# Optimization experiments

Measured on AMD Instinct MI355X. Metric: run time of the kernel, lower is better.

The kernel has to match this reference:

```python
import jax, jax.numpy as jnp
import numpy as np

W_DIM = 512
CHANNELS = 1024
SIZE = 64            # H = W = 64
SAMPLING_RATE = 64.0
BANDWIDTH = 2.0


def setup_inputs() -> dict:
    key = jax.random.key(0)
    k_w, k_f, k_p, k_wt, k_aw = jax.random.split(key, 5)
    B = 16
    w = jax.random.normal(k_w, (B, W_DIM), dtype=jnp.float32)
    # freqs init as in SynthesisInput.__init__
    freqs = jax.random.normal(k_f, (CHANNELS, 2), dtype=jnp.float32)
    radii = jnp.sqrt(jnp.sum(freqs ** 2, axis=1, keepdims=True))
    freqs = freqs / (radii * jnp.exp(radii ** 2) ** 0.25) * BANDWIDTH
    phases = jax.random.uniform(k_p, (CHANNELS,), dtype=jnp.float32) - 0.5
    weight = jax.random.normal(k_wt, (CHANNELS, CHANNELS), dtype=jnp.float32)
    # affine FC layer (weight_init=0 in original; use small random for a useful test)
    affine_w = jax.random.normal(k_aw, (4, W_DIM), dtype=jnp.float32) * 0.1
    affine_b = jnp.array([1.0, 0.0, 0.0, 0.0], dtype=jnp.float32)
    return {"w": w, "freqs": freqs, "phases": phases, "weight": weight,
            "affine_w": affine_w, "affine_b": affine_b}


def _forward(w, freqs, phases, weight, affine_w, affine_b):
    B = w.shape[0]
    C = freqs.shape[0]
    H = Wd = SIZE
    # affine: FullyConnectedLayer gain = 1/sqrt(in_features)
    t = w @ affine_w.T / jnp.sqrt(jnp.float32(W_DIM)) + affine_b  # [B,4]
    t = t / jnp.linalg.norm(t[:, :2], axis=1, keepdims=True)
    c, s = t[:, 0], t[:, 1]
    # rotation block of m_r (identity base transform, so transform_ = m_r @ m_t)
    R = jnp.stack([jnp.stack([c, -s], -1), jnp.stack([s, c], -1)], -2)  # [B,2,2]
    # translation column: transform_[:, :2, 2] = R @ (-t[:,2:4])
    trans_col = -jnp.einsum('bij,bj->bi', R, t[:, 2:4])                 # [B,2]
    phases_b = phases[None, :] + jnp.einsum('cd,bd->bc', freqs, trans_col)  # [B,C]
    freqs_b = jnp.einsum('cd,bde->bce', freqs, R)                           # [B,C,2]
    amps = jnp.clip(
        1.0 - (jnp.linalg.norm(freqs_b, axis=2) - BANDWIDTH)
        / (SAMPLING_RATE / 2 - BANDWIDTH), 0.0, 1.0)                        # [B,C]
    # affine_grid (align_corners=False): normalized coords (2i+1)/N - 1, scaled
    sx = 0.5 * Wd / SAMPLING_RATE
    sy = 0.5 * H / SAMPLING_RATE
    u = ((jnp.arange(Wd, dtype=jnp.float32) + 0.5) / Wd * 2.0 - 1.0) * sx  # x (width)
    v = ((jnp.arange(H, dtype=jnp.float32) + 0.5) / H * 2.0 - 1.0) * sy    # y (height)
    grid = jnp.stack(jnp.meshgrid(u, v, indexing='xy'), axis=-1)           # [H,W,2]
    x = jnp.einsum('hwd,bcd->bhwc', grid, freqs_b) + phases_b[:, None, None, :]
    x = jnp.sin(x * (2.0 * jnp.pi)) * amps[:, None, None, :]
    x = jnp.einsum('bhwc,kc->bhwk', x, weight / jnp.sqrt(jnp.float32(C)))
    return jnp.transpose(x, (0, 3, 1, 2))  # [B,C,H,W]


def reference(w, freqs, phases, weight, affine_w, affine_b):
    return _forward(w, freqs, phases, weight, affine_w, affine_b)
```

## Files before the change

### kernel.cpp

```cpp
#include <hip/hip_runtime.h>

typedef __attribute__((ext_vector_type(4))) float f32x4;
typedef __attribute__((ext_vector_type(8))) short s16x8;
typedef __attribute__((ext_vector_type(8))) unsigned short u16x8;

#define W_DIM   512
#define CHANNELS 1024
#define SPATIAL 4096
#define NB      16

__device__ inline unsigned short f2bf(float x){
  unsigned int u = __float_as_uint(x);
  u += 0x7fffu + ((u >> 16) & 1u);
  return (unsigned short)(u >> 16);
}

__device__ inline float sin2pi(float x){
  return __builtin_amdgcn_sinf(__builtin_amdgcn_fractf(x));
}
__device__ inline float cos2pi(float x){
  return __builtin_amdgcn_cosf(__builtin_amdgcn_fractf(x));
}

__device__ inline void async_load16(const unsigned short* g, unsigned short* l){
  __builtin_amdgcn_global_load_lds(
      (const __attribute__((address_space(1))) void*)g,
      (__attribute__((address_space(3))) void*)l, 16, 0, 0);
}

__global__ void sy_setup(const float* __restrict__ w, const float* __restrict__ freqs,
                         const float* __restrict__ phases, const float* __restrict__ affine_w,
                         const float* __restrict__ affine_b, float4* __restrict__ params){
  int b = blockIdx.x;
  int t = threadIdx.x;
  float p0=0.f, p1=0.f, p2=0.f, p3=0.f;
  #pragma unroll
  for (int it = 0; it < 2; ++it){
    int i = t + it*256;
    float wv = w[b*W_DIM + i];
    p0 += wv * affine_w[0*W_DIM + i];
    p1 += wv * affine_w[1*W_DIM + i];
    p2 += wv * affine_w[2*W_DIM + i];
    p3 += wv * affine_w[3*W_DIM + i];
  }
  #pragma unroll
  for (int off = 32; off >= 1; off >>= 1){
    p0 += __shfl_down(p0, off);
    p1 += __shfl_down(p1, off);
    p2 += __shfl_down(p2, off);
    p3 += __shfl_down(p3, off);
  }
  __shared__ float red[4][4];
  __shared__ float sc[4];
  int wave = t >> 6, lane = t & 63;
  if (lane == 0){ red[wave][0]=p0; red[wave][1]=p1; red[wave][2]=p2; red[wave][3]=p3; }
  __syncthreads();
  if (t == 0){
    const float inv_sq = 0.04419417382415922f;
    float tv[4];
    #pragma unroll
    for (int j=0;j<4;++j){
      float s = red[0][j]+red[1][j]+red[2][j]+red[3][j];
      tv[j] = s * inv_sq + affine_b[j];
    }
    float n  = sqrtf(tv[0]*tv[0] + tv[1]*tv[1]);
    float iv = 1.0f / n;
    float c = tv[0]*iv, s = tv[1]*iv;
    float t2 = tv[2]*iv, t3 = tv[3]*iv;
    float tcx = -(c*t2 - s*t3);
    float tcy = -(s*t2 + c*t3);
    sc[0]=c; sc[1]=s; sc[2]=tcx; sc[3]=tcy;
  }
  __syncthreads();
  float c = sc[0], s = sc[1], tcx = sc[2], tcy = sc[3];
  #pragma unroll
  for (int j = 0; j < 4; ++j){
    int ci = t + j*256;
    float f0x = freqs[ci*2], f0y = freqs[ci*2+1];
    float fx =  f0x*c + f0y*s;
    float fy = -f0x*s + f0y*c;
    float ph = phases[ci] + f0x*tcx + f0y*tcy;
    float r  = sqrtf(fx*fx + fy*fy);
    float amp = 1.0f - (r - 2.0f) * (1.0f/30.0f);
    amp = fminf(fmaxf(amp, 0.0f), 1.0f);
    float4 P; P.x=fx; P.y=fy; P.z=ph; P.w=amp;
    params[b*CHANNELS + ci] = P;
  }
}

__global__ void sy_cvtw(const float* __restrict__ wt, unsigned short* __restrict__ Wbf){
  int i = (blockIdx.x*256 + threadIdx.x)*4;
  float4 v = *(const float4*)(wt + i);
  ushort4 o;
  o.x = f2bf(v.x*0.03125f); o.y = f2bf(v.y*0.03125f);
  o.z = f2bf(v.z*0.03125f); o.w = f2bf(v.w*0.03125f);
  *(ushort4*)(Wbf + i) = o;
}

__global__ void sy_genS(const float4* __restrict__ params, unsigned short* __restrict__ Sbf,
                        int b0){
  int blk = blockIdx.x;
  int bb  = blk >> 7;
  int b   = b0 + bb;
  int m0  = (blk & 127) * 32;
  int t   = threadIdx.x;
  int c0  = (t & 127) * 8;
  int mh  = t >> 7;
  int h   = m0 >> 6;
  int w0  = (m0 + mh*16) & 63;
  float v  = (h  + 0.5f) * (1.0f/64.0f) - 0.5f;
  float u0 = (w0 + 0.5f) * (1.0f/64.0f) - 0.5f;

  float sU[8], cU[8], sV[8], cV[8], sD[8], cD[8];
  #pragma unroll
  for (int j = 0; j < 8; ++j){
    float4 P = params[b*CHANNELS + c0 + j];
    float V = v*P.y + P.z;
    sV[j] = sin2pi(V) * P.w;
    cV[j] = cos2pi(V) * P.w;
    float U = u0*P.x;
    sU[j] = sin2pi(U);
    cU[j] = cos2pi(U);
    float D = P.x * (1.0f/64.0f);
    sD[j] = sin2pi(D);
    cD[j] = cos2pi(D);
  }

  unsigned short* dst = Sbf + ((size_t)bb * SPATIAL + m0 + mh*16) * CHANNELS + c0;
  for (int im = 0; im < 16; ++im){
    u16x8 o;
    #pragma unroll
    for (int j = 0; j < 8; ++j){
      float val = sU[j]*cV[j] + cU[j]*sV[j];
      o[j] = f2bf(val);
      float ns = sU[j]*cD[j] + cU[j]*sD[j];
      float nc = cU[j]*cD[j] - sU[j]*sD[j];
      sU[j] = ns; cU[j] = nc;
    }
    *(u16x8*)(dst + (size_t)im * CHANNELS) = o;
  }
}

__global__ __launch_bounds__(256) void sy_gemm(const unsigned short* __restrict__ Wbf,
                                               const unsigned short* __restrict__ Sbf,
                                               float* __restrict__ out, int b0){
  __shared__ unsigned short lA[128*64];
  __shared__ unsigned short lB[128*64];
  const int nt = blockIdx.x, mt = blockIdx.y, bb = blockIdx.z;
  const int b = b0 + bb;
  const int tid  = threadIdx.x;
  const int lane = tid & 63, wave = tid >> 6;
  const int wm = wave & 1, wn = wave >> 1;
  const int Mbase = mt * 128, Nbase = nt * 128;

  int voff[4];
  int loff[4];
  #pragma unroll
  for (int j = 0; j < 4; ++j){
    int p   = (wave*4 + j)*64 + lane;
    int row = p >> 3;
    int kc  = (p & 7) ^ (row & 7);
    voff[j] = row*CHANNELS + kc*8;
    loff[j] = p*8;
  }
  const unsigned short* Abase = Wbf + (size_t)Mbase * CHANNELS;
  const unsigned short* Bbase = Sbf + ((size_t)bb*SPATIAL + Nbase) * CHANNELS;

  f32x4 acc[4][4];
  #pragma unroll
  for (int i=0;i<4;++i)
    #pragma unroll
    for (int j=0;j<4;++j){
      f32x4 z = {0.f,0.f,0.f,0.f};
      acc[i][j] = z;
    }

  const int r7 = lane & 7;
  const int rbA = (wm*64 + (lane & 15))*64;
  const int rbB = (wn*64 + (lane & 15))*64;
  const int x0 = (((lane >> 4)    ) ^ r7) * 8;
  const int x1 = (((lane >> 4) + 4) ^ r7) * 8;

  for (int kt = 0; kt < 16; ++kt){
    const int ko = kt * 64;
    #pragma unroll
    for (int j = 0; j < 4; ++j){
      async_load16(Abase + voff[j] + ko, lA + loff[j]);
      async_load16(Bbase + voff[j] + ko, lB + loff[j]);
    }
    __syncthreads();
    #pragma unroll
    for (int ks = 0; ks < 2; ++ks){
      const int xo = ks ? x1 : x0;
      s16x8 af[4], bv[4];
      #pragma unroll
      for (int i=0;i<4;++i) af[i] = *(const s16x8*)&lA[rbA + i*1024 + xo];
      #pragma unroll
      for (int j=0;j<4;++j) bv[j] = *(const s16x8*)&lB[rbB + j*1024 + xo];
      #pragma unroll
      for (int i=0;i<4;++i)
        #pragma unroll
        for (int j=0;j<4;++j)
          acc[i][j] = __builtin_amdgcn_mfma_f32_16x16x32_bf16(af[i], bv[j], acc[i][j], 0, 0, 0);
    }
    __syncthreads();
  }

  float* outb = out + (size_t)b * CHANNELS * SPATIAL;
  const int col  = Nbase + wn*64 + (lane & 15);
  const int row0 = Mbase + wm*64 + ((lane >> 4) << 2);
  #pragma unroll
  for (int i=0;i<4;++i)
    #pragma unroll
    for (int j=0;j<4;++j)
      #pragma unroll
      for (int r=0;r<4;++r)
        outb[(size_t)(row0 + i*16 + r) * SPATIAL + (col + j*16)] = acc[i][j][r];
}

__global__ void sy_fallback(const float* __restrict__ weight, const float4* __restrict__ params,
                            float* __restrict__ out){
  extern __shared__ float S[];
  int b  = blockIdx.x >> 7;
  int m0 = (blockIdx.x & 127) * 32;
  int t  = threadIdx.x;
  {
    int c0 = t*4;
    float4 P0 = params[b*CHANNELS+c0+0], P1 = params[b*CHANNELS+c0+1];
    float4 P2 = params[b*CHANNELS+c0+2], P3 = params[b*CHANNELS+c0+3];
    int h = m0 >> 6;
    float v = (h + 0.5f)*(1.0f/64.0f) - 0.5f;
    float a0 = v*P0.y+P0.z, a1 = v*P1.y+P1.z, a2 = v*P2.y+P2.z, a3 = v*P3.y+P3.z;
    for (int im = 0; im < 32; ++im){
      int wv = (m0+im) & 63;
      float u = (wv+0.5f)*(1.0f/64.0f) - 0.5f;
      float* row = S + im*CHANNELS + c0;
      row[0] = sin2pi(u*P0.x+a0)*P0.w;
      row[1] = sin2pi(u*P1.x+a1)*P1.w;
      row[2] = sin2pi(u*P2.x+a2)*P2.w;
      row[3] = sin2pi(u*P3.x+a3)*P3.w;
    }
  }
  __syncthreads();
  for (int oi = t; oi < 32*1024; oi += 256){
    int k = oi >> 5, im = oi & 31;
    const float4* wr = (const float4*)(weight + (size_t)k*CHANNELS);
    const float4* sr = (const float4*)(S + im*CHANNELS);
    float sum = 0.f;
    for (int c4 = 0; c4 < CHANNELS/4; ++c4){
      float4 a = wr[c4], s4 = sr[c4];
      sum += a.x*s4.x + a.y*s4.y + a.z*s4.z + a.w*s4.w;
    }
    out[((size_t)b*CHANNELS + k)*SPATIAL + m0 + im] = sum * 0.03125f;
  }
}

extern "C" void kernel_launch(void* const* d_in, const int* in_sizes, int n_in,
                              void* d_out, int out_size, void* d_ws, size_t ws_size,
                              hipStream_t stream){
  const float* w        = (const float*)d_in[0];
  const float* freqs    = (const float*)d_in[1];
  const float* phases   = (const float*)d_in[2];
  const float* weight   = (const float*)d_in[3];
  const float* affine_w = (const float*)d_in[4];
  const float* affine_b = (const float*)d_in[5];
  float* out = (float*)d_out;

  char* ws = (char*)d_ws;
  float4* params = (float4*)ws;
  const size_t off_w = 262144;
  const size_t off_s = off_w + 2097152;
  unsigned short* Wbf = (unsigned short*)(ws + off_w);
  unsigned short* Sbf = (unsigned short*)(ws + off_s);
  const size_t per_batch = (size_t)SPATIAL * CHANNELS * 2;

  sy_setup<<<NB, 256, 0, stream>>>(w, freqs, phases, affine_w, affine_b, params);

  int G = 0;
  if (ws_size >= off_s + per_batch){
    size_t avail = (ws_size - off_s) / per_batch;
    G = avail >= (size_t)NB ? NB : (int)avail;
  }
  if (G == 0){
    sy_fallback<<<NB*128, 256, 32*1024*4, stream>>>(weight, params, out);
    return;
  }
  sy_cvtw<<<1024, 256, 0, stream>>>(weight, Wbf);
  for (int b0 = 0; b0 < NB; b0 += G){
    int g = (NB - b0) < G ? (NB - b0) : G;
    sy_genS<<<g*128, 256, 0, stream>>>(params, Sbf, b0);
    dim3 grid(32, 8, g);
    sy_gemm<<<grid, 256, 0, stream>>>(Wbf, Sbf, out, b0);
  }
}
```

Before: 476.4 us.

## Rewrite GEMM with 256x256 tiles, double-buffered LDS and XCD-aware block remap

Replaces the 128x128 single-buffered GEMM with a 512-thread, 256x256-tile kernel. It double-buffers LDS so global loads for the next K-step are issued while MFMAs run on the current one, using explicit vmcnt/lgkmcnt waits, barriers and setprio. Block IDs are remapped across XCDs, and a 1D grid covers all batches. The larger tile raises register and LDS pressure (128 KB LDS, 128 accumulator floats per thread), which may limit occupancy.

```diff
diff --git a/kernel.cpp b/kernel.cpp
--- a/kernel.cpp
+++ b/kernel.cpp
@@ -141,81 +141,151 @@
   }
 }
 
-__global__ __launch_bounds__(256) void sy_gemm(const unsigned short* __restrict__ Wbf,
-                                               const unsigned short* __restrict__ Sbf,
-                                               float* __restrict__ out, int b0){
-  __shared__ unsigned short lA[128*64];
-  __shared__ unsigned short lB[128*64];
-  const int nt = blockIdx.x, mt = blockIdx.y, bb = blockIdx.z;
-  const int b = b0 + bb;
+__global__ __launch_bounds__(512, 2) void sy_gemm(const unsigned short* __restrict__ Wbf,
+                                                  const unsigned short* __restrict__ Sbf,
+                                                  float* __restrict__ out, int b0){
+  __shared__ __align__(16) unsigned short lds[2][2][16384];
   const int tid  = threadIdx.x;
   const int lane = tid & 63, wave = tid >> 6;
-  const int wm = wave & 1, wn = wave >> 1;
-  const int Mbase = mt * 128, Nbase = nt * 128;
-
-  int voff[4];
-  int loff[4];
-  #pragma unroll
-  for (int j = 0; j < 4; ++j){
-    int p   = (wave*4 + j)*64 + lane;
-    int row = p >> 3;
-    int kc  = (p & 7) ^ (row & 7);
-    voff[j] = row*CHANNELS + kc*8;
-    loff[j] = p*8;
-  }
-  const unsigned short* Abase = Wbf + (size_t)Mbase * CHANNELS;
-  const unsigned short* Bbase = Sbf + ((size_t)bb*SPATIAL + Nbase) * CHANNELS;
-
-  f32x4 acc[4][4];
-  #pragma unroll
-  for (int i=0;i<4;++i)
+  const int wm = wave >> 2, wn = wave & 3;
+
+  const int nwg = gridDim.x;
+  const int cpx = nwg >> 3;
+  const int bid = blockIdx.x;
+  const int sbid = (bid & 7)*cpx + (bid >> 3);
+  const int mt  = sbid & 3;
+  const int ntl = sbid >> 2;
+  const size_t NcolL = (size_t)ntl * 256;
+  const int bbl = (int)(NcolL >> 12);
+  const int nin = (int)(NcolL & 4095);
+  const unsigned short* Abase = Wbf + (size_t)mt * 256 * CHANNELS;
+  const unsigned short* Bbase = Sbf + NcolL * CHANNELS;
+
+  const int srow = tid >> 3;
+  const int cg   = (tid & 7) ^ (srow & 7);
+  const int goff = srow*CHANNELS + cg*8;
+  const int lof  = tid*8;
+
+#define STG(buf, base, op, u, ko) \
+  async_load16((base) + (size_t)((u)*64)*CHANNELS + goff + (ko), \
+               &lds[buf][op][(u)*4096 + lof])
+
+  const int l15 = lane & 15, kg = lane >> 4;
+  const int ck0 = ((kg    ) ^ (l15 & 7))*8;
+  const int ck1 = ((kg + 4) ^ (l15 & 7))*8;
+  const int arow = (wm*128 + l15)*64;
+  const int brow = (wn*64  + l15)*64;
+
+  f32x4 acc[8][4];
+  #pragma unroll
+  for (int i=0;i<8;++i)
     #pragma unroll
     for (int j=0;j<4;++j){
       f32x4 z = {0.f,0.f,0.f,0.f};
       acc[i][j] = z;
     }
 
-  const int r7 = lane & 7;
-  const int rbA = (wm*64 + (lane & 15))*64;
-  const int rbB = (wn*64 + (lane & 15))*64;
-  const int x0 = (((lane >> 4)    ) ^ r7) * 8;
-  const int x1 = (((lane >> 4) + 4) ^ r7) * 8;
-
-  for (int kt = 0; kt < 16; ++kt){
-    const int ko = kt * 64;
+  s16x8 af[4], bv0[4], bv1[4];
+
+#define DS_AF(cur, mh, CK) \
+  af[0]=*(const s16x8*)&lds[cur][0][arow + ((mh)*64+ 0)*64 + (CK)]; \
+  af[1]=*(const s16x8*)&lds[cur][0][arow + ((mh)*64+16)*64 + (CK)]; \
+  af[2]=*(const s16x8*)&lds[cur][0][arow + ((mh)*64+32)*64 + (CK)]; \
+  af[3]=*(const s16x8*)&lds[cur][0][arow + ((mh)*64+48)*64 + (CK)];
+#define DS_BV(cur, BV, CK) \
+  BV[0]=*(const s16x8*)&lds[cur][1][brow +  0*64 + (CK)]; \
+  BV[1]=*(const s16x8*)&lds[cur][1][brow + 16*64 + (CK)]; \
+  BV[2]=*(const s16x8*)&lds[cur][1][brow + 32*64 + (CK)]; \
+  BV[3]=*(const s16x8*)&lds[cur][1][brow + 48*64 + (CK)];
+#define MFMA16(mh, BV) \
+  __builtin_amdgcn_s_setprio(1); \
+  _Pragma("unroll") \
+  for (int mf=0; mf<4; ++mf){ \
+    _Pragma("unroll") \
+    for (int nf=0; nf<4; ++nf) \
+      acc[(mh)*4+mf][nf] = __builtin_amdgcn_mfma_f32_16x16x32_bf16(af[mf], BV[nf], acc[(mh)*4+mf][nf], 0, 0, 0); \
+  } \
+  __builtin_amdgcn_s_setprio(0);
+#define LGKM0 \
+  asm volatile("s_waitcnt lgkmcnt(0)" ::: "memory"); \
+  __builtin_amdgcn_sched_barrier(0);
+
+  STG(0, Bbase, 1, 0, 0); STG(0, Abase, 0, 0, 0);
+  STG(0, Bbase, 1, 1, 0); STG(0, Abase, 0, 2, 0);
+  STG(0, Bbase, 1, 2, 0); STG(0, Bbase, 1, 3, 0);
+  STG(0, Abase, 0, 1, 0); STG(0, Abase, 0, 3, 0);
+  asm volatile("s_waitcnt vmcnt(2)" ::: "memory");
+  __builtin_amdgcn_s_barrier();
+
+  for (int T = 0; T < 15; ++T){
+    const int cur = T & 1, nxt = cur ^ 1;
+    const int ko = (T+1)*64;
+    DS_AF(cur, 0, ck0); DS_BV(cur, bv0, ck0);
+    STG(nxt, Bbase, 1, 0, ko); STG(nxt, Abase, 0, 0, ko);
+    STG(nxt, Bbase, 1, 1, ko); STG(nxt, Abase, 0, 2, ko);
+    __builtin_amdgcn_s_barrier();
+    LGKM0;
+    MFMA16(0, bv0);
+    __builtin_amdgcn_s_barrier();
+    DS_AF(cur, 0, ck1); DS_BV(cur, bv1, ck1);
+    STG(nxt, Bbase, 1, 2, ko); STG(nxt, Bbase, 1, 3, ko);
+    STG(nxt, Abase, 0, 1, ko); STG(nxt, Abase, 0, 3, ko);
+    __builtin_amdgcn_s_barrier();
+    LGKM0;
+    MFMA16(0, bv1);
+    asm volatile("s_waitcnt vmcnt(6)" ::: "memory");
+    __builtin_amdgcn_s_barrier();
+    DS_AF(cur, 1, ck0);
+    __builtin_amdgcn_s_barrier();
+    LGKM0;
+    MFMA16(1, bv0);
+    __builtin_amdgcn_s_barrier();
+    DS_AF(cur, 1, ck1);
+    __builtin_amdgcn_s_barrier();
+    LGKM0;
+    MFMA16(1, bv1);
+    asm volatile("s_waitcnt vmcnt(2)" ::: "memory");
+    __builtin_amdgcn_s_barrier();
+  }
+  {
+    const int cur = 1;
+    DS_AF(cur, 0, ck0); DS_BV(cur, bv0, ck0);
+    __builtin_amdgcn_s_barrier();
+    LGKM0;
+    MFMA16(0, bv0);
+    __builtin_amdgcn_s_barrier();
+    DS_AF(cur, 0, ck1); DS_BV(cur, bv1, ck1);
+    __builtin_amdgcn_s_barrier();
+    LGKM0;
+    MFMA16(0, bv1);
+    asm volatile("s_waitcnt vmcnt(0)" ::: "memory");
+    __builtin_amdgcn_s_barrier();
+    DS_AF(cur, 1, ck0);
+    __builtin_amdgcn_s_barrier();
+    LGKM0;
+    MFMA16(1, bv0);
+    __builtin_amdgcn_s_barrier();
+    DS_AF(cur, 1, ck1);
+    __builtin_amdgcn_s_barrier();
+    LGKM0;
+    MFMA16(1, bv1);
+  }
+
+  float* outb = out + (size_t)(b0 + bbl) * CHANNELS * SPATIAL;
+  const int colb = nin + wn*64 + l15;
+  const int row0 = mt*256 + wm*128 + (kg << 2);
+  #pragma unroll
+  for (int mf = 0; mf < 8; ++mf)
     #pragma unroll
-    for (int j = 0; j < 4; ++j){
-      async_load16(Abase + voff[j] + ko, lA + loff[j]);
-      async_load16(Bbase + voff[j] + ko, lB + loff[j]);
-    }
-    __syncthreads();
-    #pragma unroll
-    for (int ks = 0; ks < 2; ++ks){
-      const int xo = ks ? x1 : x0;
-      s16x8 af[4], bv[4];
+    for (int nf = 0; nf < 4; ++nf)
       #pragma unroll
-      for (int i=0;i<4;++i) af[i] = *(const s16x8*)&lA[rbA + i*1024 + xo];
-      #pragma unroll
-      for (int j=0;j<4;++j) bv[j] = *(const s16x8*)&lB[rbB + j*1024 + xo];
-      #pragma unroll
-      for (int i=0;i<4;++i)
-        #pragma unroll
-        for (int j=0;j<4;++j)
-          acc[i][j] = __builtin_amdgcn_mfma_f32_16x16x32_bf16(af[i], bv[j], acc[i][j], 0, 0, 0);
-    }
-    __syncthreads();
-  }
-
-  float* outb = out + (size_t)b * CHANNELS * SPATIAL;
-  const int col  = Nbase + wn*64 + (lane & 15);
-  const int row0 = Mbase + wm*64 + ((lane >> 4) << 2);
-  #pragma unroll
-  for (int i=0;i<4;++i)
-    #pragma unroll
-    for (int j=0;j<4;++j)
-      #pragma unroll
-      for (int r=0;r<4;++r)
-        outb[(size_t)(row0 + i*16 + r) * SPATIAL + (col + j*16)] = acc[i][j][r];
+      for (int r = 0; r < 4; ++r)
+        outb[(size_t)(row0 + mf*16 + r) * SPATIAL + colb + nf*16] = acc[mf][nf][r];
+#undef STG
+#undef DS_AF
+#undef DS_BV
+#undef MFMA16
+#undef LGKM0
 }
 
 __global__ void sy_fallback(const float* __restrict__ weight, const float4* __restrict__ params,
@@ -289,7 +359,6 @@
   for (int b0 = 0; b0 < NB; b0 += G){
     int g = (NB - b0) < G ? (NB - b0) : G;
     sy_genS<<<g*128, 256, 0, stream>>>(params, Sbf, b0);
-    dim3 grid(32, 8, g);
-    sy_gemm<<<grid, 256, 0, stream>>>(Wbf, Sbf, out, b0);
-  }
-}
+    sy_gemm<<<g*64, 512, 0, stream>>>(Wbf, Sbf, out, b0);
+  }
+}
```

Result: faster. 432.0 us (-9.3%).

## Rewrite bf16 GEMM with 256x128 tiles, triple-buffered LDS pipeline and XCD remap

Applied to the files above, without the earlier changes.

The GEMM kernel now uses 512-thread blocks that each compute a 256x128 output tile, stepping through K in chunks of 32. A three-stage LDS ring lets async global loads for later stages overlap with MFMA work on the current stage, and the per-step double __syncthreads is replaced by one vmcnt wait plus a barrier. A 1-D grid with an XCD-aware block remap and raised MFMA priority via s_setprio are meant to improve L2 locality and issue scheduling. The trade-offs are more LDS per block and a fixed assumption that the grid size is a multiple of 8.

```diff
diff --git a/kernel.cpp b/kernel.cpp
--- a/kernel.cpp
+++ b/kernel.cpp
@@ -141,30 +141,48 @@
   }
 }
 
-__global__ __launch_bounds__(256) void sy_gemm(const unsigned short* __restrict__ Wbf,
-                                               const unsigned short* __restrict__ Sbf,
-                                               float* __restrict__ out, int b0){
-  __shared__ unsigned short lA[128*64];
-  __shared__ unsigned short lB[128*64];
-  const int nt = blockIdx.x, mt = blockIdx.y, bb = blockIdx.z;
-  const int b = b0 + bb;
+__global__ __launch_bounds__(512, 4) void sy_gemm(const unsigned short* __restrict__ Wbf,
+                                                  const unsigned short* __restrict__ Sbf,
+                                                  float* __restrict__ out, int b0){
+  __shared__ __align__(16) unsigned short lds[3][12288];
   const int tid  = threadIdx.x;
   const int lane = tid & 63, wave = tid >> 6;
-  const int wm = wave & 1, wn = wave >> 1;
-  const int Mbase = mt * 128, Nbase = nt * 128;
-
-  int voff[4];
-  int loff[4];
-  #pragma unroll
-  for (int j = 0; j < 4; ++j){
-    int p   = (wave*4 + j)*64 + lane;
-    int row = p >> 3;
-    int kc  = (p & 7) ^ (row & 7);
-    voff[j] = row*CHANNELS + kc*8;
-    loff[j] = p*8;
-  }
-  const unsigned short* Abase = Wbf + (size_t)Mbase * CHANNELS;
-  const unsigned short* Bbase = Sbf + ((size_t)bb*SPATIAL + Nbase) * CHANNELS;
+  const int wm = wave >> 1, wn = wave & 1;
+
+  const int nwg = gridDim.x;
+  const int cpx = nwg >> 3;
+  const int bid = blockIdx.x;
+  const int sbid = (bid & 7)*cpx + (bid >> 3);
+  const int mt  = sbid & 3;
+  const int ntl = sbid >> 2;
+  const size_t NcolL = (size_t)ntl * 128;
+  const int bbl = (int)(NcolL >> 12);
+  const int nin = (int)(NcolL & 4095);
+  const unsigned short* Abase = Wbf + (size_t)mt * 256 * CHANNELS;
+  const unsigned short* Bbase = Sbf + NcolL * CHANNELS;
+
+  int voffA[2], loffA[2];
+  #pragma unroll
+  for (int j = 0; j < 2; ++j){
+    int p   = j*512 + tid;
+    int row = p >> 2;
+    int kc  = (p & 3) ^ ((row >> 1) & 3);
+    voffA[j] = row*CHANNELS + kc*8;
+    loffA[j] = p*8;
+  }
+  int voffB, loffB;
+  {
+    int p   = tid;
+    int row = p >> 2;
+    int kc  = (p & 3) ^ ((row >> 1) & 3);
+    voffB   = row*CHANNELS + kc*8;
+    loffB   = 8192 + p*8;
+  }
+
+  const int l15 = lane & 15, kg = lane >> 4;
+  const int xs  = (kg ^ ((l15 >> 1) & 3)) * 8;
+  const int aoff =        (wm*64 + l15)*32 + xs;
+  const int boff = 8192 + (wn*64 + l15)*32 + xs;
 
   f32x4 acc[4][4];
   #pragma unroll
@@ -175,47 +193,57 @@
       acc[i][j] = z;
     }
 
-  const int r7 = lane & 7;
-  const int rbA = (wm*64 + (lane & 15))*64;
-  const int rbB = (wn*64 + (lane & 15))*64;
-  const int x0 = (((lane >> 4)    ) ^ r7) * 8;
-  const int x1 = (((lane >> 4) + 4) ^ r7) * 8;
-
-  for (int kt = 0; kt < 16; ++kt){
-    const int ko = kt * 64;
-    #pragma unroll
-    for (int j = 0; j < 4; ++j){
-      async_load16(Abase + voff[j] + ko, lA + loff[j]);
-      async_load16(Bbase + voff[j] + ko, lB + loff[j]);
-    }
-    __syncthreads();
-    #pragma unroll
-    for (int ks = 0; ks < 2; ++ks){
-      const int xo = ks ? x1 : x0;
-      s16x8 af[4], bv[4];
+  auto STAGE = [&](int kt, int s){
+    const int ko = kt * 32;
+    unsigned short* l = &lds[s][0];
+    async_load16(Abase + voffA[0] + ko, l + loffA[0]);
+    async_load16(Abase + voffA[1] + ko, l + loffA[1]);
+    async_load16(Bbase + voffB   + ko, l + loffB);
+  };
+  auto COMPUTE = [&](int s){
+    const unsigned short* l = &lds[s][0];
+    s16x8 af[4], bv[4];
+    #pragma unroll
+    for (int i=0;i<4;++i) af[i] = *(const s16x8*)&l[aoff + i*512];
+    #pragma unroll
+    for (int j=0;j<4;++j) bv[j] = *(const s16x8*)&l[boff + j*512];
+    __builtin_amdgcn_s_setprio(1);
+    #pragma unroll
+    for (int i=0;i<4;++i)
       #pragma unroll
-      for (int i=0;i<4;++i) af[i] = *(const s16x8*)&lA[rbA + i*1024 + xo];
+      for (int j=0;j<4;++j)
+        acc[i][j] = __builtin_amdgcn_mfma_f32_16x16x32_bf16(af[i], bv[j], acc[i][j], 0, 0, 0);
+    __builtin_amdgcn_s_setprio(0);
+  };
+
+  STAGE(0, 0); STAGE(1, 1);
+  asm volatile("s_waitcnt vmcnt(3)" ::: "memory");
+  __builtin_amdgcn_s_barrier();
+
+  int sc = 0, ss = 2;
+  for (int t = 0; t < 30; ++t){
+    STAGE(t + 2, ss);
+    COMPUTE(sc);
+    asm volatile("s_waitcnt vmcnt(3)" ::: "memory");
+    __builtin_amdgcn_s_barrier();
+    sc = (sc == 2) ? 0 : sc + 1;
+    ss = (ss == 2) ? 0 : ss + 1;
+  }
+  COMPUTE(sc);
+  asm volatile("s_waitcnt vmcnt(0)" ::: "memory");
+  __builtin_amdgcn_s_barrier();
+  COMPUTE(1);
+
+  float* outb = out + (size_t)(b0 + bbl) * CHANNELS * SPATIAL;
+  const int colb = nin + wn*64 + l15;
+  const int row0 = mt*256 + wm*64 + (kg << 2);
+  #pragma unroll
+  for (int mf = 0; mf < 4; ++mf)
+    #pragma unroll
+    for (int nf = 0; nf < 4; ++nf)
       #pragma unroll
-      for (int j=0;j<4;++j) bv[j] = *(const s16x8*)&lB[rbB + j*1024 + xo];
-      #pragma unroll
-      for (int i=0;i<4;++i)
-        #pragma unroll
-        for (int j=0;j<4;++j)
-          acc[i][j] = __builtin_amdgcn_mfma_f32_16x16x32_bf16(af[i], bv[j], acc[i][j], 0, 0, 0);
-    }
-    __syncthreads();
-  }
-
-  float* outb = out + (size_t)b * CHANNELS * SPATIAL;
-  const int col  = Nbase + wn*64 + (lane & 15);
-  const int row0 = Mbase + wm*64 + ((lane >> 4) << 2);
-  #pragma unroll
-  for (int i=0;i<4;++i)
-    #pragma unroll
-    for (int j=0;j<4;++j)
-      #pragma unroll
-      for (int r=0;r<4;++r)
-        outb[(size_t)(row0 + i*16 + r) * SPATIAL + (col + j*16)] = acc[i][j][r];
+      for (int r = 0; r < 4; ++r)
+        outb[(size_t)(row0 + mf*16 + r) * SPATIAL + colb + nf*16] = acc[mf][nf][r];
 }
 
 __global__ void sy_fallback(const float* __restrict__ weight, const float4* __restrict__ params,
@@ -289,7 +317,6 @@
   for (int b0 = 0; b0 < NB; b0 += G){
     int g = (NB - b0) < G ? (NB - b0) : G;
     sy_genS<<<g*128, 256, 0, stream>>>(params, Sbf, b0);
-    dim3 grid(32, 8, g);
-    sy_gemm<<<grid, 256, 0, stream>>>(Wbf, Sbf, out, b0);
-  }
-}
+    sy_gemm<<<g*128, 512, 0, stream>>>(Wbf, Sbf, out, b0);
+  }
+}
```

After: 439.3 us. -7.8%, faster.
